# Performance work log

Measured on AMD Instinct MI355X. Metric: run time of the kernel, lower is better.

## Reference

```python
import jax, jax.numpy as jnp
import numpy as np

B, L, N = 64, 64, 32           # programs, statement trees per program, nodes per tree
V, E, C, H, OUT = 100000, 128, 128, 100, 104
MAX_DEPTH = 10


def setup_inputs() -> dict:
    key = jax.random.key(0)
    ks = jax.random.split(key, 14)
    rng = np.random.default_rng(0)
    num_trees = B * L
    T = num_trees * N
    # random trees: parent index < node index, depth capped at MAX_DEPTH
    par = np.zeros((num_trees, N), np.int64)
    lev = np.zeros((num_trees, N), np.int64)
    for i in range(1, N):
        p = rng.integers(0, i, size=num_trees)
        pl = lev[np.arange(num_trees), p]
        too_deep = pl + 1 > MAX_DEPTH
        p = np.where(too_deep, 0, p)
        lev[:, i] = np.where(too_deep, 1, pl + 1)
        par[:, i] = p
    base = (np.arange(num_trees) * N)[:, None]
    parent = jnp.asarray((par + base).reshape(-1))          # global parent index
    level = jnp.asarray(lev.reshape(-1))
    tree_id = jnp.asarray(np.repeat(np.arange(num_trees), N))
    node_ids = jax.random.randint(ks[0], (T,), 0, V)
    r = lambda k, shape, s=0.05: (jax.random.normal(k, shape) * s).astype(jnp.float32)
    return {
        'node_ids': node_ids, 'parent': parent, 'level': level, 'tree_id': tree_id,
        'emb': r(ks[1], (V, E), 1.0),
        'W_lin': r(ks[2], (E, C)), 'b_lin': r(ks[3], (C,)),
        'w_ih_f': r(ks[4], (3 * H, C)), 'w_hh_f': r(ks[5], (3 * H, H)),
        'b_ih_f': r(ks[6], (3 * H,)), 'b_hh_f': r(ks[7], (3 * H,)),
        'w_ih_b': r(ks[8], (3 * H, C)), 'w_hh_b': r(ks[9], (3 * H, H)),
        'b_ih_b': r(ks[10], (3 * H,)), 'b_hh_b': r(ks[11], (3 * H,)),
        'fc_w': r(ks[12], (2 * H, OUT)), 'fc_b': r(ks[13], (OUT,)),
    }


def _run_gru(xs, wih, whh, bih, bhh, reverse):
    # xs: [L, B, C]; torch GRU gate math
    def step(hprev, x):
        gi = x @ wih.T + bih
        gh = hprev @ whh.T + bhh
        ir, iz, inn = jnp.split(gi, 3, axis=-1)
        hr, hz, hn = jnp.split(gh, 3, axis=-1)
        rg = jax.nn.sigmoid(ir + hr)
        zg = jax.nn.sigmoid(iz + hz)
        ng = jnp.tanh(inn + rg * hn)
        hnew = (1.0 - zg) * ng + zg * hprev
        return hnew, hnew
    h0 = jnp.zeros((xs.shape[1], whh.shape[1]), xs.dtype)
    _, out = jax.lax.scan(step, h0, xs, reverse=reverse)
    return out  # [L, B, H]


def _forward(node_ids, parent, level, tree_id, emb, W_lin, b_lin,
             w_ih_f, w_hh_f, b_ih_f, b_hh_f, w_ih_b, w_hh_b, b_ih_b, b_hh_b,
             fc_w, fc_b):
    # per-node: h = W*emb(id) + b, then child-sum bottom-up by depth level
    h = emb[node_ids] @ W_lin + b_lin            # [T, C]
    for d in range(MAX_DEPTH, 0, -1):
        contrib = jnp.where((level == d)[:, None], h, 0.0)
        h = h.at[parent].add(contrib)
    # per-tree max pool over all node hidden states -> statement vectors
    stmt = jax.ops.segment_max(h, tree_id, num_segments=B * L)  # [B*L, C]
    xs = stmt.reshape(B, L, C).transpose(1, 0, 2)               # [L, B, C]
    out_f = _run_gru(xs, w_ih_f, w_hh_f, b_ih_f, b_hh_f, reverse=False)
    out_b = _run_gru(xs, w_ih_b, w_hh_b, b_ih_b, b_hh_b, reverse=True)
    gru_out = jnp.concatenate([out_f, out_b], axis=-1)          # [L, B, 2H]
    pooled = gru_out.max(axis=0)                                # [B, 2H]
    return pooled @ fc_w + fc_b                                 # [B, OUT]


def reference(node_ids, parent, level, tree_id, emb, W_lin, b_lin,
              w_ih_f, w_hh_f, b_ih_f, b_hh_f, w_ih_b, w_hh_b, b_ih_b, b_hh_b,
              fc_w, fc_b):
    return _forward(node_ids, parent, level, tree_id, emb, W_lin, b_lin,
                    w_ih_f, w_hh_f, b_ih_f, b_hh_f, w_ih_b, w_hh_b, b_ih_b, b_hh_b,
                    fc_w, fc_b)
```

## Files before the change

### kernel.cpp

```cpp
#include <hip/hip_runtime.h>

typedef _Float16 half8 __attribute__((ext_vector_type(8)));
typedef float f32x4 __attribute__((ext_vector_type(4)));
typedef float f32x16 __attribute__((ext_vector_type(16)));

union H8 { half8 h; float4 f; };

#define EDIM 128
#define CDIM 128
#define HDIM 100
#define ODIM 104

#define OFF_WFRAG  0u
#define OFF_WIH    32768u
#define OFF_WHH    204800u
#define OFF_BIASP  376832u
#define OFF_STMT   379904u
#define OFF_POOL   1428480u

__device__ inline f32x4 zero4() { f32x4 z = {0.f, 0.f, 0.f, 0.f}; return z; }

__device__ inline float fast_exp2(float x) {
  float r; asm("v_exp_f32 %0, %1" : "=v"(r) : "v"(x)); return r;
}
__device__ inline float fast_rcp(float x) {
  float r; asm("v_rcp_f32 %0, %1" : "=v"(r) : "v"(x)); return r;
}
__device__ inline float sigmoid_f(float x) {
  return fast_rcp(1.f + fast_exp2(x * -1.44269504f));
}
__device__ inline float tanh_f(float x) {
  float e = fast_exp2(x * 2.88539008f);
  return fmaf(fast_rcp(1.f + e), -2.f, 1.f);
}

#define HSWZ(row) ((((row) & 3) << 4) ^ (((row) & 12) << 3))

__global__ __launch_bounds__(256) void astnn_prep(
    const float* __restrict__ W_lin,
    const float* __restrict__ wihf, const float* __restrict__ whhf,
    const float* __restrict__ bihf, const float* __restrict__ bhhf,
    const float* __restrict__ wihb, const float* __restrict__ whhb,
    const float* __restrict__ bihb, const float* __restrict__ bhhb,
    _Float16* __restrict__ wfrag, _Float16* __restrict__ wihfrag,
    _Float16* __restrict__ whhfrag, float* __restrict__ biasP)
{
  int gid = blockIdx.x * 256 + threadIdx.x;
  if (gid < 2048) {
    int i = gid, l = i & 63, kc = (i >> 6) & 3, nt = i >> 8;
    int n = (nt << 4) + (l & 15);
    int kb = (kc << 5) + ((l >> 4) << 3);
#pragma unroll
    for (int e = 0; e < 8; e++)
      wfrag[i * 8 + e] = (_Float16)W_lin[(kb + e) * CDIM + n];
  } else if (gid < 12800) {
    int i = gid - 2048, l = i & 63, kc = (i >> 6) & 3;
    int rest = i >> 8, nt = rest % 21, d = rest / 21;
    const float* wih = d ? wihb : wihf;
    int n = (nt << 4) + (l & 15), s = n / 112, j = n - 112 * s;
    int kb = (kc << 5) + ((l >> 4) << 3);
#pragma unroll
    for (int e = 0; e < 8; e++) {
      int k = kb + e;
      float v = (j < HDIM) ? wih[(s * HDIM + j) * CDIM + k] : 0.f;
      wihfrag[i * 8 + e] = (_Float16)v;
    }
  } else if (gid < 23552) {
    int i = gid - 12800, l = i & 63, kc = (i >> 6) & 3;
    int rest = i >> 8, nt = rest % 21, d = rest / 21;
    const float* whh = d ? whhb : whhf;
    const float* bhh = d ? bhhb : bhhf;
    int n = (nt << 4) + (l & 15), s = n / 112, j = n - 112 * s;
    int kb = (kc << 5) + ((l >> 4) << 3);
#pragma unroll
    for (int e = 0; e < 8; e++) {
      int k = kb + e;
      float v = 0.f;
      if (j < HDIM) {
        if (k < HDIM) v = whh[(s * HDIM + j) * HDIM + k];
        else if (k == HDIM && s == 2) v = bhh[2 * HDIM + j];
      }
      whhfrag[i * 8 + e] = (_Float16)v;
    }
  } else if (gid < 24320) {
    int i = gid - 23552, d = i / 384, col = i % 384, s = col >> 7, j = col & 127;
    const float* bih = d ? bihb : bihf;
    const float* bhh = d ? bhhb : bhhf;
    float v = 0.f;
    if (j < HDIM) { v = bih[s * HDIM + j]; if (s < 2) v += bhh[s * HDIM + j]; }
    biasP[i] = v;
  }
}

__global__ __launch_bounds__(256, 2) void astnn_tree(
    const int* __restrict__ node_ids, const int* __restrict__ parent,
    const float* __restrict__ emb, const float* __restrict__ b_lin,
    const _Float16* __restrict__ wfrag, _Float16* __restrict__ stmt)
{
  __shared__ _Float16 ldsW[16384];
  __shared__ _Float16 ldsA[16384];
  __shared__ int ldsPar[128];
  __shared__ unsigned ldsAnc[128];

  const int t = threadIdx.x, blk = blockIdx.x;
  const int w = t >> 6, l = t & 63;
  const int base = blk * 128;

  if (t < 128) ldsPar[t] = parent[base + t] & 31;

  {
    const float4* wsrc = (const float4*)wfrag;
#pragma unroll
    for (int i = 0; i < 8; i++) ((float4*)ldsW)[i * 256 + t] = wsrc[i * 256 + t];
  }

  {
    const int r = t >> 1, hf = t & 1;
    const int nid = node_ids[base + r];
    const float4* erow = (const float4*)(emb + (size_t)nid * EDIM) + hf * 16;
#pragma unroll
    for (int b2 = 0; b2 < 2; b2++) {
      float4 stage[8];
#pragma unroll
      for (int i = 0; i < 8; i++) stage[i] = erow[b2 * 8 + i];
#pragma unroll
      for (int c4 = 0; c4 < 4; c4++) {
        H8 u;
#pragma unroll
        for (int e = 0; e < 8; e++)
          u.h[e] = (_Float16)(((const float*)&stage[0])[c4 * 8 + e]);
        int c = b2 * 4 + c4;
        int addr = (r * 256 + hf * 128 + c * 16) ^ ((r & 7) << 4);
        *(float4*)((char*)ldsA + addr) = u.f;
      }
    }
  }
  __syncthreads();

  if (t < 128) {
    int tree = t >> 5;
    unsigned mask = 0;
    int cur = t & 31;
#pragma unroll
    for (int it = 0; it < 11; ++it) { mask |= (1u << cur); cur = ldsPar[tree * 32 + cur]; }
    ldsAnc[t] = mask;
  }
  __syncthreads();

  f32x4 acc[2][8];
#pragma unroll
  for (int mt = 0; mt < 2; mt++)
#pragma unroll
    for (int nt = 0; nt < 8; nt++) acc[mt][nt] = zero4();
#pragma unroll
  for (int kc = 0; kc < 4; kc++) {
    half8 af[2];
#pragma unroll
    for (int mt = 0; mt < 2; mt++) {
      int row = (w * 2 + mt) * 16 + (l & 15);
      int addr = (row * 256 + (kc << 6) + ((l >> 4) << 4)) ^ ((row & 7) << 4);
      af[mt] = *(const half8*)((const char*)ldsA + addr);
    }
#pragma unroll
    for (int nt = 0; nt < 8; nt++) {
      half8 bf = *(const half8*)&ldsW[(((nt << 2) | kc) * 64 + l) * 8];
      acc[0][nt] = __builtin_amdgcn_mfma_f32_16x16x32_f16(af[0], bf, acc[0][nt], 0, 0, 0);
      acc[1][nt] = __builtin_amdgcn_mfma_f32_16x16x32_f16(af[1], bf, acc[1][nt], 0, 0, 0);
    }
  }
  __syncthreads();

#pragma unroll
  for (int mt = 0; mt < 2; mt++) {
    const int Mt = w * 2 + mt, tree = Mt >> 1, kc2 = Mt & 1;
#pragma unroll
    for (int nt = 0; nt < 8; nt++) {
      const float bl = b_lin[nt * 16 + (l & 15)];
      const int nt2 = nt >> 1;
      const int ncol = ((nt & 1) << 4) + (l & 15);
#pragma unroll
      for (int reg = 0; reg < 4; reg++) {
        int rowrem = ((l >> 4) << 2) + reg;
        int l2 = ((rowrem >> 3) << 5) + ncol;
        int idx = (((((tree << 2) + nt2) << 1) + kc2) * 64 + l2) * 8 + (rowrem & 7);
        ldsA[idx] = (_Float16)(acc[mt][nt][reg] + bl);
      }
    }
  }
  __syncthreads();

  {
    const int tree = w;
    half8 ancf[2];
#pragma unroll
    for (int kc2 = 0; kc2 < 2; kc2++) {
      H8 u;
#pragma unroll
      for (int e = 0; e < 8; e++) {
        int n = (kc2 << 4) + ((l >> 5) << 3) + e;
        unsigned m = ldsAnc[(tree << 5) + n];
        u.h[e] = (_Float16)(float)((m >> (l & 31)) & 1u);
      }
      ancf[kc2] = u.h;
    }
    f32x16 acc2[4];
#pragma unroll
    for (int nt2 = 0; nt2 < 4; nt2++)
#pragma unroll
      for (int e = 0; e < 16; e++) acc2[nt2][e] = 0.f;
#pragma unroll
    for (int nt2 = 0; nt2 < 4; nt2++)
#pragma unroll
      for (int kc2 = 0; kc2 < 2; kc2++) {
        half8 bf = *(const half8*)&ldsA[(((((tree << 2) + nt2) << 1) + kc2) * 64 + l) * 8];
        acc2[nt2] = __builtin_amdgcn_mfma_f32_32x32x16_f16(ancf[kc2], bf, acc2[nt2], 0, 0, 0);
      }
#pragma unroll
    for (int nt2 = 0; nt2 < 4; nt2++) {
      float m1 = acc2[nt2][0];
#pragma unroll
      for (int e = 1; e < 16; e++) m1 = fmaxf(m1, acc2[nt2][e]);
      m1 = fmaxf(m1, __shfl_xor(m1, 32));
      if (l < 32) {
        int g = blk * 4 + tree;
        int rowp = (g & 63) * 64 + (g >> 6);
        stmt[(size_t)rowp * CDIM + (nt2 << 5) + l] = (_Float16)m1;
      }
    }
  }
}

__global__ __launch_bounds__(448) void astnn_gru(
    const _Float16* __restrict__ whhfrag, const _Float16* __restrict__ wihfrag,
    const _Float16* __restrict__ stmt, const float* __restrict__ biasP,
    float* __restrict__ pooled)
{
  __shared__ _Float16 hlds[4096];
  const int t = threadIdx.x, w = t >> 6, l = t & 63;
  const int mb = blockIdx.x, dir = blockIdx.y;
  for (int i = t; i < 512; i += 448)
    ((float4*)hlds)[i] = make_float4(0.f, 0.f, 0.f, 0.f);
  __syncthreads();
  if (t < 32) {
    int row = t & 15, buf = t >> 4;
    int addr = ((row * 256 + 200) ^ HSWZ(row)) + (buf << 12);
    *(_Float16*)((char*)hlds + addr) = (_Float16)1.0f;
  }

  const int j = (w << 4) + (l & 15);
  const bool jv = (j < HDIM);
  const int rloc = (l >> 4) << 2;
  const int grow = (mb << 4) + rloc;

  int raddr[4], waddr[4];
  {
    int row = l & 15;
#pragma unroll
    for (int kc = 0; kc < 4; kc++)
      raddr[kc] = (row * 256 + (kc << 6) + ((l >> 4) << 4)) ^ HSWZ(row);
#pragma unroll
    for (int reg = 0; reg < 4; reg++) {
      int rw = rloc + reg;
      waddr[reg] = (rw * 256 + (j << 1)) ^ HSWZ(rw);
    }
  }

  half8 bfr[3][4], bfw[3][4];
  {
    const half8* wfh = (const half8*)whhfrag + dir * 5376;
    const half8* wfi = (const half8*)wihfrag + dir * 5376;
#pragma unroll
    for (int s = 0; s < 3; s++)
#pragma unroll
      for (int kc = 0; kc < 4; kc++) {
        int idx = (((s * 7 + w) << 2) + kc) * 64 + l;
        bfr[s][kc] = wfh[idx];
        bfw[s][kc] = wfi[idx];
      }
  }
  const float bias0 = biasP[dir * 384 + j];
  const float bias1 = biasP[dir * 384 + 128 + j];
  const float bias2 = biasP[dir * 384 + 256 + j];

  int soff[4];
#pragma unroll
  for (int kc = 0; kc < 4; kc++)
    soff[kc] = (((mb << 4) + (l & 15)) * 256) + (kc << 6) + ((l >> 4) << 4);
  const ptrdiff_t sstep = dir ? -16384 : 16384;
  const char* sbase = (const char*)stmt + (size_t)(dir ? 63 : 0) * 16384;

  half8 sfA[4], sfB[4];
#pragma unroll
  for (int kc = 0; kc < 4; kc++) sfA[kc] = *(const half8*)(sbase + soff[kc]);
  const char* spre = sbase + sstep;
#pragma unroll
  for (int kc = 0; kc < 4; kc++) sfB[kc] = *(const half8*)(spre + soff[kc]);
  spre += sstep;

  f32x4 giA[3], giB[3];
  giA[0] = f32x4{bias0, bias0, bias0, bias0};
  giA[1] = f32x4{bias1, bias1, bias1, bias1};
  giA[2] = f32x4{bias2, bias2, bias2, bias2};
#pragma unroll
  for (int kc = 0; kc < 4; kc++) {
    giA[0] = __builtin_amdgcn_mfma_f32_16x16x32_f16(sfA[kc], bfw[0][kc], giA[0], 0, 0, 0);
    giA[1] = __builtin_amdgcn_mfma_f32_16x16x32_f16(sfA[kc], bfw[1][kc], giA[1], 0, 0, 0);
    giA[2] = __builtin_amdgcn_mfma_f32_16x16x32_f16(sfA[kc], bfw[2][kc], giA[2], 0, 0, 0);
  }

  float hreg[4], pool[4];
#pragma unroll
  for (int i = 0; i < 4; i++) { hreg[i] = 0.f; pool[i] = -3.0e38f; }
  __syncthreads();

#define GRU_BODY(GIC, GIN, SFsrc, SFdst, ROFF, WOFF, CN, PF)                    \
  {                                                                             \
    half8 afh[4];                                                               \
    _Pragma("unroll")                                                           \
    for (int kc = 0; kc < 4; kc++)                                              \
      afh[kc] = *(const half8*)((const char*)hlds + raddr[kc] + (ROFF));        \
    f32x4 acc0 = GIC[0], acc1 = GIC[1];                                         \
    f32x4 acc2i = GIC[2], acc2h = zero4();                                      \
    if (CN) {      \
      GIN[0] = f32x4{bias0, bias0, bias0, bias0};                               \
      GIN[1] = f32x4{bias1, bias1, bias1, bias1};                               \
      GIN[2] = f32x4{bias2, bias2, bias2, bias2};                               \
      _Pragma("unroll")                                                         \
      for (int kc = 0; kc < 4; kc++) {                                          \
        GIN[0] = __builtin_amdgcn_mfma_f32_16x16x32_f16(SFsrc[kc], bfw[0][kc], GIN[0], 0, 0, 0); \
        GIN[1] = __builtin_amdgcn_mfma_f32_16x16x32_f16(SFsrc[kc], bfw[1][kc], GIN[1], 0, 0, 0); \
        GIN[2] = __builtin_amdgcn_mfma_f32_16x16x32_f16(SFsrc[kc], bfw[2][kc], GIN[2], 0, 0, 0); \
      }                                                                         \
    }                                                                           \
    if (PF) {                                                                   \
      SFdst[0] = *(const half8*)(spre + soff[0]);                               \
      SFdst[1] = *(const half8*)(spre + soff[1]);                               \
      SFdst[2] = *(const half8*)(spre + soff[2]);                               \
      SFdst[3] = *(const half8*)(spre + soff[3]);                               \
      spre += sstep;                                                            \
    }                                                                           \
    _Pragma("unroll")                                                           \
    for (int kc = 0; kc < 4; kc++) {                                            \
      acc0  = __builtin_amdgcn_mfma_f32_16x16x32_f16(afh[kc], bfr[0][kc], acc0, 0, 0, 0); \
      acc1  = __builtin_amdgcn_mfma_f32_16x16x32_f16(afh[kc], bfr[1][kc], acc1, 0, 0, 0); \
      acc2h = __builtin_amdgcn_mfma_f32_16x16x32_f16(afh[kc], bfr[2][kc], acc2h, 0, 0, 0);\
    }                                                                           \
    _Pragma("unroll")                                                           \
    for (int reg = 0; reg < 4; reg++) {                                         \
      float r = sigmoid_f(acc0[reg]);                                           \
      float z = sigmoid_f(acc1[reg]);                                           \
      float n = tanh_f(fmaf(r, acc2h[reg], acc2i[reg]));                        \
      float hn = n + z * (hreg[reg] - n);                                       \
      hreg[reg] = hn;                                                           \
      pool[reg] = fmaxf(pool[reg], hn);                                         \
      if (jv)                                                                   \
        *(_Float16*)((char*)hlds + waddr[reg] + (WOFF)) = (_Float16)hn;         \
    }                                                                           \
    asm volatile("s_waitcnt lgkmcnt(0)" ::: "memory");                          \
    __builtin_amdgcn_s_barrier();                                               \
    __builtin_amdgcn_sched_barrier(0);                                          \
  }

#pragma unroll 1
  for (int it = 0; it < 31; ++it) {
    GRU_BODY(giA, giB, sfB, sfA, 0, 4096, 1, 1)
    GRU_BODY(giB, giA, sfA, sfB, 4096, 0, 1, 1)
  }
  GRU_BODY(giA, giB, sfB, sfA, 0, 4096, 1, 0)
  GRU_BODY(giB, giA, sfA, sfB, 4096, 0, 0, 0)
#undef GRU_BODY

  if (jv) {
#pragma unroll
    for (int reg = 0; reg < 4; reg++)
      pooled[((size_t)dir << 13) + ((size_t)(grow + reg) << 7) + j] = pool[reg];
  }
}

__global__ __launch_bounds__(128) void astnn_fc(
    const float* __restrict__ pooled, const float* __restrict__ fc_w,
    const float* __restrict__ fc_b, float* __restrict__ out)
{
  __shared__ float p[200];
  const int b = blockIdx.x, t = threadIdx.x;
  for (int i = t; i < 200; i += 128) {
    int d = i / 100, jj = i - d * 100;
    p[i] = pooled[((size_t)d << 13) + (b << 7) + jj];
  }
  __syncthreads();
  if (t < ODIM) {
    float a = fc_b[t];
#pragma unroll 8
    for (int k = 0; k < 200; k++) a = fmaf(p[k], fc_w[k * ODIM + t], a);
    out[b * ODIM + t] = a;
  }
}

extern "C" void kernel_launch(void* const* d_in, const int* in_sizes, int n_in,
                              void* d_out, int out_size, void* d_ws, size_t ws_size,
                              hipStream_t stream)
{
  const int* node_ids = (const int*)d_in[0];
  const int* parent   = (const int*)d_in[1];
  const float* emb    = (const float*)d_in[4];
  const float* W_lin  = (const float*)d_in[5];
  const float* b_lin  = (const float*)d_in[6];
  const float* wihf   = (const float*)d_in[7];
  const float* whhf   = (const float*)d_in[8];
  const float* bihf   = (const float*)d_in[9];
  const float* bhhf   = (const float*)d_in[10];
  const float* wihb   = (const float*)d_in[11];
  const float* whhb   = (const float*)d_in[12];
  const float* bihb   = (const float*)d_in[13];
  const float* bhhb   = (const float*)d_in[14];
  const float* fc_w   = (const float*)d_in[15];
  const float* fc_b   = (const float*)d_in[16];

  char* ws = (char*)d_ws;
  _Float16* wfrag   = (_Float16*)(ws + OFF_WFRAG);
  _Float16* wihfrag = (_Float16*)(ws + OFF_WIH);
  _Float16* whhfrag = (_Float16*)(ws + OFF_WHH);
  float* biasP      = (float*)(ws + OFF_BIASP);
  _Float16* stmt    = (_Float16*)(ws + OFF_STMT);
  float* pooled     = (float*)(ws + OFF_POOL);
  float* out        = (float*)d_out;

  astnn_prep<<<95, 256, 0, stream>>>(W_lin, wihf, whhf, bihf, bhhf,
                                     wihb, whhb, bihb, bhhb,
                                     wfrag, wihfrag, whhfrag, biasP);
  astnn_tree<<<1024, 256, 0, stream>>>(node_ids, parent, emb, b_lin, wfrag, stmt);
  astnn_gru<<<dim3(4, 2), 448, 0, stream>>>(whhfrag, wihfrag, stmt, biasP, pooled);
  astnn_fc<<<64, 128, 0, stream>>>(pooled, fc_w, fc_b, out);
}
```

Measured before the change: 88.95 us.

## Fuse weight-prep kernel into tree kernel and reorder GRU MFMA issue

Removes the separate astnn_prep launch. The first 87 tree blocks now build the GRU input/hidden weight fragments and biases, and every tree block converts W_lin straight into its LDS fragment layout instead of copying a precomputed fragment buffer. This saves one kernel launch and its serialization, but each of the 1024 blocks now does strided fp32 reads and conversions of W_lin. In the GRU step, the recurrent h·Whh MFMAs are issued before the next step's input-projection MFMAs, so the dependent gate math can start sooner.

```diff
diff --git a/kernel.cpp b/kernel.cpp
--- a/kernel.cpp
+++ b/kernel.cpp
@@ -11,7 +11,6 @@
 #define HDIM 100
 #define ODIM 104
 
-#define OFF_WFRAG  0u
 #define OFF_WIH    32768u
 #define OFF_WHH    204800u
 #define OFF_BIASP  376832u
@@ -36,66 +35,16 @@
 
 #define HSWZ(row) ((((row) & 3) << 4) ^ (((row) & 12) << 3))
 
-__global__ __launch_bounds__(256) void astnn_prep(
-    const float* __restrict__ W_lin,
+__global__ __launch_bounds__(256, 2) void astnn_tree(
+    const int* __restrict__ node_ids, const int* __restrict__ parent,
+    const float* __restrict__ emb, const float* __restrict__ W_lin,
+    const float* __restrict__ b_lin,
     const float* __restrict__ wihf, const float* __restrict__ whhf,
     const float* __restrict__ bihf, const float* __restrict__ bhhf,
     const float* __restrict__ wihb, const float* __restrict__ whhb,
     const float* __restrict__ bihb, const float* __restrict__ bhhb,
-    _Float16* __restrict__ wfrag, _Float16* __restrict__ wihfrag,
-    _Float16* __restrict__ whhfrag, float* __restrict__ biasP)
-{
-  int gid = blockIdx.x * 256 + threadIdx.x;
-  if (gid < 2048) {
-    int i = gid, l = i & 63, kc = (i >> 6) & 3, nt = i >> 8;
-    int n = (nt << 4) + (l & 15);
-    int kb = (kc << 5) + ((l >> 4) << 3);
-#pragma unroll
-    for (int e = 0; e < 8; e++)
-      wfrag[i * 8 + e] = (_Float16)W_lin[(kb + e) * CDIM + n];
-  } else if (gid < 12800) {
-    int i = gid - 2048, l = i & 63, kc = (i >> 6) & 3;
-    int rest = i >> 8, nt = rest % 21, d = rest / 21;
-    const float* wih = d ? wihb : wihf;
-    int n = (nt << 4) + (l & 15), s = n / 112, j = n - 112 * s;
-    int kb = (kc << 5) + ((l >> 4) << 3);
-#pragma unroll
-    for (int e = 0; e < 8; e++) {
-      int k = kb + e;
-      float v = (j < HDIM) ? wih[(s * HDIM + j) * CDIM + k] : 0.f;
-      wihfrag[i * 8 + e] = (_Float16)v;
-    }
-  } else if (gid < 23552) {
-    int i = gid - 12800, l = i & 63, kc = (i >> 6) & 3;
-    int rest = i >> 8, nt = rest % 21, d = rest / 21;
-    const float* whh = d ? whhb : whhf;
-    const float* bhh = d ? bhhb : bhhf;
-    int n = (nt << 4) + (l & 15), s = n / 112, j = n - 112 * s;
-    int kb = (kc << 5) + ((l >> 4) << 3);
-#pragma unroll
-    for (int e = 0; e < 8; e++) {
-      int k = kb + e;
-      float v = 0.f;
-      if (j < HDIM) {
-        if (k < HDIM) v = whh[(s * HDIM + j) * HDIM + k];
-        else if (k == HDIM && s == 2) v = bhh[2 * HDIM + j];
-      }
-      whhfrag[i * 8 + e] = (_Float16)v;
-    }
-  } else if (gid < 24320) {
-    int i = gid - 23552, d = i / 384, col = i % 384, s = col >> 7, j = col & 127;
-    const float* bih = d ? bihb : bihf;
-    const float* bhh = d ? bhhb : bhhf;
-    float v = 0.f;
-    if (j < HDIM) { v = bih[s * HDIM + j]; if (s < 2) v += bhh[s * HDIM + j]; }
-    biasP[i] = v;
-  }
-}
-
-__global__ __launch_bounds__(256, 2) void astnn_tree(
-    const int* __restrict__ node_ids, const int* __restrict__ parent,
-    const float* __restrict__ emb, const float* __restrict__ b_lin,
-    const _Float16* __restrict__ wfrag, _Float16* __restrict__ stmt)
+    _Float16* __restrict__ wihfrag, _Float16* __restrict__ whhfrag,
+    float* __restrict__ biasP, _Float16* __restrict__ stmt)
 {
   __shared__ _Float16 ldsW[16384];
   __shared__ _Float16 ldsA[16384];
@@ -106,12 +55,60 @@
   const int w = t >> 6, l = t & 63;
   const int base = blk * 128;
 
+  if (blk < 87) {
+    int gid = blk * 256 + t;
+    if (gid < 10752) {
+      int i = gid, ll = i & 63, kc = (i >> 6) & 3;
+      int rest = i >> 8, nt = rest % 21, d = rest / 21;
+      const float* wih = d ? wihb : wihf;
+      int n = (nt << 4) + (ll & 15), s = n / 112, j = n - 112 * s;
+      int kb = (kc << 5) + ((ll >> 4) << 3);
+#pragma unroll
+      for (int e = 0; e < 8; e++) {
+        int k = kb + e;
+        float v = (j < HDIM) ? wih[(s * HDIM + j) * CDIM + k] : 0.f;
+        wihfrag[i * 8 + e] = (_Float16)v;
+      }
+    } else if (gid < 21504) {
+      int i = gid - 10752, ll = i & 63, kc = (i >> 6) & 3;
+      int rest = i >> 8, nt = rest % 21, d = rest / 21;
+      const float* whh = d ? whhb : whhf;
+      const float* bhh = d ? bhhb : bhhf;
+      int n = (nt << 4) + (ll & 15), s = n / 112, j = n - 112 * s;
+      int kb = (kc << 5) + ((ll >> 4) << 3);
+#pragma unroll
+      for (int e = 0; e < 8; e++) {
+        int k = kb + e;
+        float v = 0.f;
+        if (j < HDIM) {
+          if (k < HDIM) v = whh[(s * HDIM + j) * HDIM + k];
+          else if (k == HDIM && s == 2) v = bhh[2 * HDIM + j];
+        }
+        whhfrag[i * 8 + e] = (_Float16)v;
+      }
+    } else {
+      int i = gid - 21504, d = i / 384, col = i % 384, s = col >> 7, j = col & 127;
+      const float* bih = d ? bihb : bihf;
+      const float* bhh = d ? bhhb : bhhf;
+      float v = 0.f;
+      if (j < HDIM) { v = bih[s * HDIM + j]; if (s < 2) v += bhh[s * HDIM + j]; }
+      biasP[i] = v;
+    }
+  }
+
   if (t < 128) ldsPar[t] = parent[base + t] & 31;
 
   {
-    const float4* wsrc = (const float4*)wfrag;
-#pragma unroll
-    for (int i = 0; i < 8; i++) ((float4*)ldsW)[i * 256 + t] = wsrc[i * 256 + t];
+#pragma unroll
+    for (int i8 = 0; i8 < 8; i8++) {
+      int fi = i8 * 256 + t;
+      int ll = fi & 63, kc = (fi >> 6) & 3, nt = fi >> 8;
+      int n = (nt << 4) + (ll & 15);
+      int kb = (kc << 5) + ((ll >> 4) << 3);
+#pragma unroll
+      for (int e = 0; e < 8; e++)
+        ldsW[fi * 8 + e] = (_Float16)W_lin[(kb + e) * CDIM + n];
+    }
   }
 
   {
@@ -321,7 +318,13 @@
       afh[kc] = *(const half8*)((const char*)hlds + raddr[kc] + (ROFF));        \
     f32x4 acc0 = GIC[0], acc1 = GIC[1];                                         \
     f32x4 acc2i = GIC[2], acc2h = zero4();                                      \
-    if (CN) {      \
+    _Pragma("unroll")                             \
+    for (int kc = 0; kc < 4; kc++) {                                            \
+      acc0  = __builtin_amdgcn_mfma_f32_16x16x32_f16(afh[kc], bfr[0][kc], acc0, 0, 0, 0); \
+      acc1  = __builtin_amdgcn_mfma_f32_16x16x32_f16(afh[kc], bfr[1][kc], acc1, 0, 0, 0); \
+      acc2h = __builtin_amdgcn_mfma_f32_16x16x32_f16(afh[kc], bfr[2][kc], acc2h, 0, 0, 0);\
+    }                                                                           \
+    if (CN) {     \
       GIN[0] = f32x4{bias0, bias0, bias0, bias0};                               \
       GIN[1] = f32x4{bias1, bias1, bias1, bias1};                               \
       GIN[2] = f32x4{bias2, bias2, bias2, bias2};                               \
@@ -338,12 +341,6 @@
       SFdst[2] = *(const half8*)(spre + soff[2]);                               \
       SFdst[3] = *(const half8*)(spre + soff[3]);                               \
       spre += sstep;                                                            \
-    }                                                                           \
-    _Pragma("unroll")                                                           \
-    for (int kc = 0; kc < 4; kc++) {                                            \
-      acc0  = __builtin_amdgcn_mfma_f32_16x16x32_f16(afh[kc], bfr[0][kc], acc0, 0, 0, 0); \
-      acc1  = __builtin_amdgcn_mfma_f32_16x16x32_f16(afh[kc], bfr[1][kc], acc1, 0, 0, 0); \
-      acc2h = __builtin_amdgcn_mfma_f32_16x16x32_f16(afh[kc], bfr[2][kc], acc2h, 0, 0, 0);\
     }                                                                           \
     _Pragma("unroll")                                                           \
     for (int reg = 0; reg < 4; reg++) {                                         \
@@ -417,7 +414,6 @@
   const float* fc_b   = (const float*)d_in[16];
 
   char* ws = (char*)d_ws;
-  _Float16* wfrag   = (_Float16*)(ws + OFF_WFRAG);
   _Float16* wihfrag = (_Float16*)(ws + OFF_WIH);
   _Float16* whhfrag = (_Float16*)(ws + OFF_WHH);
   float* biasP      = (float*)(ws + OFF_BIASP);
@@ -425,10 +421,10 @@
   float* pooled     = (float*)(ws + OFF_POOL);
   float* out        = (float*)d_out;
 
-  astnn_prep<<<95, 256, 0, stream>>>(W_lin, wihf, whhf, bihf, bhhf,
-                                     wihb, whhb, bihb, bhhb,
-                                     wfrag, wihfrag, whhfrag, biasP);
-  astnn_tree<<<1024, 256, 0, stream>>>(node_ids, parent, emb, b_lin, wfrag, stmt);
+  astnn_tree<<<1024, 256, 0, stream>>>(node_ids, parent, emb, W_lin, b_lin,
+                                       wihf, whhf, bihf, bhhf,
+                                       wihb, whhb, bihb, bhhb,
+                                       wihfrag, whhfrag, biasP, stmt);
   astnn_gru<<<dim3(4, 2), 448, 0, stream>>>(whhfrag, wihfrag, stmt, biasP, pooled);
   astnn_fc<<<64, 128, 0, stream>>>(pooled, fc_w, fc_b, out);
 }
```

Measured after the change: 85.74 us. 1.04x faster.
